# Optimization experiments

Hardware: AMD Instinct MI355X
Metric: run time of the kernel (lower is better)

## Reference

```python
import math
import jax, jax.numpy as jnp
import numpy as np

B, N, ND, CD, H, L, T = 2, 384, 8, 16, 128, 4, 100

def silu(x):
    return x * jax.nn.sigmoid(x)

def mlp2(x, w1, b1, w2, b2):
    return silu(x @ w1 + b1) @ w2 + b2

def setup_inputs() -> dict:
    key = jax.random.key(0)
    ks = iter(jax.random.split(key, 80))
    def nrm(shape, scale=1.0):
        return jax.random.normal(next(ks), shape, jnp.float32) * scale
    def lin(fi, fo):
        s = 1.0 / np.sqrt(fi)
        return nrm((fi, fo), s), nrm((fo,), s)
    def stack_lin(fi, fo):
        ws, bs = zip(*[lin(fi, fo) for _ in range(L)])
        return jnp.stack(ws), jnp.stack(bs)
    inp = {}
    inp['node_features'] = nrm((B, N, ND))
    inp['positions'] = nrm((B, N, 2))
    inp['mask'] = jnp.ones((B, N), jnp.float32)
    inp['condition'] = nrm((B, CD))
    inp['targets'] = nrm((B, 4))
    inp['property_weights'] = jax.random.uniform(next(ks), (4,), jnp.float32)
    inp['feature_noise'] = nrm((B, N, ND))
    inp['position_noise'] = nrm((B, N, 2))
    inp['timesteps'] = jax.random.randint(next(ks), (B,), 0, T)
    inp['time_w1'], inp['time_b1'] = lin(H, H)
    inp['time_w2'], inp['time_b2'] = lin(H, H)
    inp['cond_w1'], inp['cond_b1'] = lin(CD, H)
    inp['cond_w2'], inp['cond_b2'] = lin(H, H)
    inp['nodep_w1'], inp['nodep_b1'] = lin(ND + 2, H)
    inp['nodep_w2'], inp['nodep_b2'] = lin(H, H)
    inp['edge_w1'], inp['edge_b1'] = stack_lin(2 * H + 1, H)
    inp['edge_w2'], inp['edge_b2'] = stack_lin(H, H)
    inp['nodem_w1'], inp['nodem_b1'] = stack_lin(2 * H, H)
    inp['nodem_w2'], inp['nodem_b2'] = stack_lin(H, H)
    inp['feat_w1'], inp['feat_b1'] = lin(H, H)
    inp['feat_w2'], inp['feat_b2'] = lin(H, ND)
    inp['pos_w1'], inp['pos_b1'] = lin(H, H)
    inp['pos_w2'], inp['pos_b2'] = lin(H, 2)
    inp['prop_w1'], inp['prop_b1'] = lin(H, H)
    inp['prop_w2'], inp['prop_b2'] = lin(H, H // 2)
    inp['prop_w3'], inp['prop_b3'] = lin(H // 2, 4)
    return inp

def reference(node_features, positions, mask, condition, targets, property_weights,
              feature_noise, position_noise, timesteps,
              time_w1, time_b1, time_w2, time_b2,
              cond_w1, cond_b1, cond_w2, cond_b2,
              nodep_w1, nodep_b1, nodep_w2, nodep_b2,
              edge_w1, edge_b1, edge_w2, edge_b2,
              nodem_w1, nodem_b1, nodem_w2, nodem_b2,
              feat_w1, feat_b1, feat_w2, feat_b2,
              pos_w1, pos_b1, pos_w2, pos_b2,
              prop_w1, prop_b1, prop_w2, prop_b2, prop_w3, prop_b3):
    # diffusion schedule buffers
    betas = jnp.linspace(1e-4, 0.02, T)
    alpha_bars = jnp.cumprod(1.0 - betas)
    ab = alpha_bars[timesteps][:, None, None]
    nf = jnp.sqrt(ab) * node_features + jnp.sqrt(1.0 - ab) * feature_noise
    npos = jnp.sqrt(ab) * positions + jnp.sqrt(1.0 - ab) * position_noise
    # sinusoidal time embedding
    half = H // 2
    factor = math.log(10000.0) / (half - 1)
    freqs = jnp.exp(jnp.arange(half) * (-factor))
    te = timesteps.astype(jnp.float32)[:, None] * freqs[None, :]
    temb = jnp.concatenate([jnp.sin(te), jnp.cos(te)], -1)
    state = (mlp2(jnp.concatenate([nf, npos], -1), nodep_w1, nodep_b1, nodep_w2, nodep_b2)
             + mlp2(temb, time_w1, time_b1, time_w2, time_b2)[:, None, :]
             + mlp2(condition, cond_w1, cond_b1, cond_w2, cond_b2)[:, None, :])
    # pairwise distances (fixed across layers); eps for grad-safe sqrt at diagonal
    rel = npos[:, :, None, :] - npos[:, None, :, :]
    dist = jnp.sqrt(jnp.sum(rel * rel, -1) + 1e-12)  # [B,N,N]
    emask = mask[:, :, None] * mask[:, None, :]       # [B,N,N]
    denom = jnp.clip(emask.sum(2), 1.0)[..., None]    # [B,N,1]
    mask3 = mask[..., None]

    def layer(s, p):
        ew1, eb1, ew2, eb2, nw1, nb1, nw2, nb2 = p
        # split first edge-linear: cat([node_i, node_j, dist]) @ ew1
        ai = s @ ew1[:H]            # [B,N,H] (i contribution)
        aj = s @ ew1[H:2 * H]       # [B,N,H] (j contribution)
        h = silu(ai[:, :, None, :] + aj[:, None, :, :] + dist[..., None] * ew1[2 * H] + eb1)
        msg = (h @ ew2 + eb2) * emask[..., None]
        agg = msg.sum(2) / denom    # [B,N,H]
        upd = silu(s @ nw1[:H] + agg @ nw1[H:] + nb1) @ nw2 + nb2
        return s + upd * mask3, None

    state, _ = jax.lax.scan(layer, state,
                            (edge_w1, edge_b1, edge_w2, edge_b2,
                             nodem_w1, nodem_b1, nodem_w2, nodem_b2))
    pred_fn = mlp2(state, feat_w1, feat_b1, feat_w2, feat_b2)
    pred_pn = mlp2(state, pos_w1, pos_b1, pos_w2, pos_b2)
    gemb = (state * mask3).sum(1) / jnp.clip(mask.sum(1, keepdims=True), 1.0)
    props = silu(silu(gemb @ prop_w1 + prop_b1) @ prop_w2 + prop_b2) @ prop_w3 + prop_b3
    msum = jnp.clip(mask.sum(), 1.0)
    floss = (((pred_fn - feature_noise) ** 2) * mask3).sum() / msum
    ploss = (((pred_pn - position_noise) ** 2) * mask3).sum() / msum
    noise_loss = floss + ploss
    prop_loss = (((props - targets) ** 2) * property_weights).mean()
    total_loss = noise_loss + prop_loss
    return jnp.stack([noise_loss, prop_loss, total_loss])
```

## Files before the change

kernel.cpp:

```cpp
#include <hip/hip_runtime.h>
#include <math.h>

#define BB 2
#define NN 384
#define ND 8
#define CD 16
#define HH 128
#define LL 4
#define TT 100
#define TOTN (BB * NN)

__device__ __forceinline__ float silu_f(float x) {
    float s = 1.0f / (1.0f + __expf(-x));
    return x * s;
}

__global__ void k_prep(const float* __restrict__ mask, const float* __restrict__ condition,
                       const int* __restrict__ timesteps,
                       const float* __restrict__ time_w1, const float* __restrict__ time_b1,
                       const float* __restrict__ time_w2, const float* __restrict__ time_b2,
                       const float* __restrict__ cond_w1, const float* __restrict__ cond_b1,
                       const float* __restrict__ cond_w2, const float* __restrict__ cond_b2,
                       float* __restrict__ tc, float* __restrict__ scal, float* __restrict__ accums) {
    int b = blockIdx.x;
    int t = threadIdx.x;
    __shared__ float sh[HH];
    __shared__ float sh2[HH];
    __shared__ float shc[CD];
    __shared__ float red[HH];

    if (b == 0 && t < 2) accums[t] = 0.0f;

    int ts = timesteps[b];
    float ab = 1.0f;
    for (int k = 0; k <= ts; ++k) {
        float beta = 1e-4f + (0.02f - 1e-4f) * ((float)k / (float)(TT - 1));
        ab *= (1.0f - beta);
    }
    if (t == 0) {
        scal[b * 4 + 0] = sqrtf(ab);
        scal[b * 4 + 1] = sqrtf(1.0f - ab);
    }
    float m = 0.0f;
    for (int j = t; j < NN; j += HH) m += mask[b * NN + j];
    red[t] = m;
    __syncthreads();
    for (int s = 64; s > 0; s >>= 1) {
        if (t < s) red[t] += red[t + s];
        __syncthreads();
    }
    if (t == 0) scal[b * 4 + 2] = red[0];

    const int half = HH / 2;
    float factor = logf(10000.0f) / (float)(half - 1);
    float tf = (float)ts;
    float temb;
    if (t < half) temb = sinf(tf * __expf(-factor * (float)t));
    else          temb = cosf(tf * __expf(-factor * (float)(t - half)));
    sh[t] = temb;
    if (t < CD) shc[t] = condition[b * CD + t];
    __syncthreads();

    float acc = time_b1[t];
    for (int k = 0; k < HH; ++k) acc += sh[k] * time_w1[k * HH + t];
    sh2[t] = silu_f(acc);
    __syncthreads();
    float acc2 = time_b2[t];
    for (int k = 0; k < HH; ++k) acc2 += sh2[k] * time_w2[k * HH + t];
    float acc3 = cond_b1[t];
    for (int k = 0; k < CD; ++k) acc3 += shc[k] * cond_w1[k * HH + t];
    __syncthreads();
    sh[t] = silu_f(acc3);
    __syncthreads();
    float acc4 = cond_b2[t];
    for (int k = 0; k < HH; ++k) acc4 += sh[k] * cond_w2[k * HH + t];

    tc[b * HH + t] = acc2 + acc4;
}

__global__ __launch_bounds__(256) void k_node_init(
    const float* __restrict__ node_features, const float* __restrict__ positions,
    const float* __restrict__ feature_noise, const float* __restrict__ position_noise,
    const float* __restrict__ nodep_w1, const float* __restrict__ nodep_b1,
    const float* __restrict__ nodep_w2, const float* __restrict__ nodep_b2,
    const float* __restrict__ tc, const float* __restrict__ scal,
    const float* __restrict__ ew1_0, const float* __restrict__ eb1_0,
    float* __restrict__ state, float* __restrict__ npos,
    float* __restrict__ ai0, float* __restrict__ aj0) {
    const int tid = threadIdx.x;
    const int t = tid & 127;
    const int g = tid >> 7;
    const int b0 = blockIdx.x * 4;
    const int b = b0 / NN;

    __shared__ __align__(16) float x[4][12];
    __shared__ __align__(16) float sh1[4][HH];
    __shared__ __align__(16) float sst[4][HH];
    __shared__ float sred[4][2][HH];

    if (tid < 40) {
        int n = tid / 10, c = tid % 10;
        int gn = b0 + n;
        float sab = scal[b * 4 + 0], s1ab = scal[b * 4 + 1];
        float v;
        if (c < ND) {
            v = sab * node_features[gn * ND + c] + s1ab * feature_noise[gn * ND + c];
        } else {
            int d = c - ND;
            v = sab * positions[gn * 2 + d] + s1ab * position_noise[gn * 2 + d];
            npos[gn * 2 + d] = v;
        }
        x[n][c] = v;
    }
    __syncthreads();

    for (int n = 2 * g; n <= 2 * g + 1; ++n) {
        float a = nodep_b1[t];
        #pragma unroll
        for (int k = 0; k < ND + 2; ++k) a += x[n][k] * nodep_w1[k * HH + t];
        sh1[n][t] = silu_f(a);
    }
    __syncthreads();

    {
        float a0 = 0, a1 = 0, a2 = 0, a3 = 0;
        const int k0 = g * 64;
        const float* wr = nodep_w2 + (size_t)k0 * HH + t;
        for (int kk = 0; kk < 64; kk += 4) {
            float w0 = wr[(kk + 0) * HH], w1 = wr[(kk + 1) * HH];
            float w2 = wr[(kk + 2) * HH], w3 = wr[(kk + 3) * HH];
            float4 s;
            s = *(const float4*)&sh1[0][k0 + kk]; a0 += s.x * w0 + s.y * w1 + s.z * w2 + s.w * w3;
            s = *(const float4*)&sh1[1][k0 + kk]; a1 += s.x * w0 + s.y * w1 + s.z * w2 + s.w * w3;
            s = *(const float4*)&sh1[2][k0 + kk]; a2 += s.x * w0 + s.y * w1 + s.z * w2 + s.w * w3;
            s = *(const float4*)&sh1[3][k0 + kk]; a3 += s.x * w0 + s.y * w1 + s.z * w2 + s.w * w3;
        }
        sred[0][g][t] = a0; sred[1][g][t] = a1; sred[2][g][t] = a2; sred[3][g][t] = a3;
    }
    __syncthreads();
    {
        float tcv = nodep_b2[t] + tc[b * HH + t];
        for (int n = 2 * g; n <= 2 * g + 1; ++n) {
            float st = sred[n][0][t] + sred[n][1][t] + tcv;
            state[(size_t)(b0 + n) * HH + t] = st;
            sst[n][t] = st;
        }
    }
    __syncthreads();

    {
        float a0 = 0, a1 = 0, a2 = 0, a3 = 0;
        const int k0 = g * 64;
        const float* wr = ew1_0 + (size_t)k0 * HH + t;
        for (int kk = 0; kk < 64; kk += 4) {
            float w0 = wr[(kk + 0) * HH], w1 = wr[(kk + 1) * HH];
            float w2 = wr[(kk + 2) * HH], w3 = wr[(kk + 3) * HH];
            float4 s;
            s = *(const float4*)&sst[0][k0 + kk]; a0 += s.x * w0 + s.y * w1 + s.z * w2 + s.w * w3;
            s = *(const float4*)&sst[1][k0 + kk]; a1 += s.x * w0 + s.y * w1 + s.z * w2 + s.w * w3;
            s = *(const float4*)&sst[2][k0 + kk]; a2 += s.x * w0 + s.y * w1 + s.z * w2 + s.w * w3;
            s = *(const float4*)&sst[3][k0 + kk]; a3 += s.x * w0 + s.y * w1 + s.z * w2 + s.w * w3;
        }
        sred[0][g][t] = a0; sred[1][g][t] = a1; sred[2][g][t] = a2; sred[3][g][t] = a3;
    }
    __syncthreads();
    for (int n = 2 * g; n <= 2 * g + 1; ++n)
        ai0[(size_t)(b0 + n) * HH + t] = sred[n][0][t] + sred[n][1][t] + eb1_0[t];
    __syncthreads();
    {
        float a0 = 0, a1 = 0, a2 = 0, a3 = 0;
        const int k0 = g * 64;
        const float* wr = ew1_0 + (size_t)(HH + k0) * HH + t;
        for (int kk = 0; kk < 64; kk += 4) {
            float w0 = wr[(kk + 0) * HH], w1 = wr[(kk + 1) * HH];
            float w2 = wr[(kk + 2) * HH], w3 = wr[(kk + 3) * HH];
            float4 s;
            s = *(const float4*)&sst[0][k0 + kk]; a0 += s.x * w0 + s.y * w1 + s.z * w2 + s.w * w3;
            s = *(const float4*)&sst[1][k0 + kk]; a1 += s.x * w0 + s.y * w1 + s.z * w2 + s.w * w3;
            s = *(const float4*)&sst[2][k0 + kk]; a2 += s.x * w0 + s.y * w1 + s.z * w2 + s.w * w3;
            s = *(const float4*)&sst[3][k0 + kk]; a3 += s.x * w0 + s.y * w1 + s.z * w2 + s.w * w3;
        }
        sred[0][g][t] = a0; sred[1][g][t] = a1; sred[2][g][t] = a2; sred[3][g][t] = a3;
    }
    __syncthreads();
    for (int n = 2 * g; n <= 2 * g + 1; ++n)
        aj0[(size_t)(b0 + n) * HH + t] = sred[n][0][t] + sred[n][1][t];
}

__global__ void k_dist(const float* __restrict__ npos, float* __restrict__ dist) {
    int idx = blockIdx.x * blockDim.x + threadIdx.x;
    if (idx >= BB * NN * NN) return;
    int b = idx / (NN * NN);
    int r = idx % (NN * NN);
    int i = r / NN, j = r % NN;
    float dx = npos[(b * NN + i) * 2 + 0] - npos[(b * NN + j) * 2 + 0];
    float dy = npos[(b * NN + i) * 2 + 1] - npos[(b * NN + j) * 2 + 1];
    dist[idx] = sqrtf(dx * dx + dy * dy + 1e-12f);
}

__global__ __launch_bounds__(256) void k_edge(
    const float* __restrict__ ai, const float* __restrict__ aj,
    const float* __restrict__ dist, const float* __restrict__ mask,
    const float* __restrict__ wd, float* __restrict__ Sp) {
    const int tid = threadIdx.x;
    const int t = tid & 127;
    const int g = tid >> 7;
    const int blk = blockIdx.x;
    const int p = blk >> 2, q = blk & 3;
    const int n0 = p * 2, n1 = p * 2 + 1;
    const int b = n0 / NN;
    const int jb = q * 96;

    __shared__ __align__(16) float4 sdm[96];
    __shared__ float sred[2][2][HH];

    for (int i = tid; i < 96; i += 256) {
        int j = jb + i;
        sdm[i] = make_float4(dist[(size_t)n0 * NN + j], dist[(size_t)n1 * NN + j],
                             mask[b * NN + j], 0.0f);
    }
    const float av0 = ai[(size_t)n0 * HH + t];
    const float av1 = ai[(size_t)n1 * HH + t];
    const float wdt = wd[t];
    __syncthreads();

    const float* pa = aj + ((size_t)b * NN + jb) * HH + t;
    float acc0 = 0.0f, acc1 = 0.0f;
    #pragma unroll 4
    for (int i = g; i < 96; i += 2) {
        float4 dm = sdm[i];
        float a = pa[(size_t)i * HH];
        float v0 = av0 + a + dm.x * wdt;
        float v1 = av1 + a + dm.y * wdt;
        acc0 = fmaf(dm.z, silu_f(v0), acc0);
        acc1 = fmaf(dm.z, silu_f(v1), acc1);
    }
    sred[0][g][t] = acc0;
    sred[1][g][t] = acc1;
    __syncthreads();
    if (g == 0) Sp[((size_t)q * TOTN + n0) * HH + t] = sred[0][0][t] + sred[0][1][t];
    else        Sp[((size_t)q * TOTN + n1) * HH + t] = sred[1][0][t] + sred[1][1][t];
}

template<bool LAST>
__global__ __launch_bounds__(256) void k_nodeup(
    const float* __restrict__ Sp, float* __restrict__ state,
    const float* __restrict__ mask, const float* __restrict__ scal,
    const float* __restrict__ ew2, const float* __restrict__ eb2,
    const float* __restrict__ nw1, const float* __restrict__ nb1,
    const float* __restrict__ nw2, const float* __restrict__ nb2,
    const float* __restrict__ ew1n, const float* __restrict__ eb1n,
    float* __restrict__ ai_out, float* __restrict__ aj_out,
    const float* __restrict__ fnoise, const float* __restrict__ pnoise,
    const float* __restrict__ fw1, const float* __restrict__ fb1,
    const float* __restrict__ fw2, const float* __restrict__ fb2,
    const float* __restrict__ pw1, const float* __restrict__ pb1,
    const float* __restrict__ pw2, const float* __restrict__ pb2,
    float* __restrict__ accums, float* __restrict__ gembp) {
    const int tid = threadIdx.x;
    const int t = tid & 127;
    const int g = tid >> 7;
    const int b0 = blockIdx.x * 4;
    const int b = b0 / NN;

    __shared__ __align__(16) float sS[4][HH];
    __shared__ __align__(16) float sst[4][HH];
    __shared__ __align__(16) float sagg[4][HH];
    __shared__ __align__(16) float sh[4][HH];
    __shared__ float sred[4][2][HH];
    __shared__ float lf, lp;

    for (int i = tid; i < 4 * HH; i += 256) {
        int n = i >> 7, tt = i & 127;
        int gn = b0 + n;
        sS[n][tt] = Sp[((size_t)0 * TOTN + gn) * HH + tt] + Sp[((size_t)1 * TOTN + gn) * HH + tt]
                  + Sp[((size_t)2 * TOTN + gn) * HH + tt] + Sp[((size_t)3 * TOTN + gn) * HH + tt];
        sst[n][tt] = state[(size_t)gn * HH + tt];
    }
    if (tid == 0) { lf = 0.0f; lp = 0.0f; }
    __syncthreads();

    {
        float a0 = 0, a1 = 0, a2 = 0, a3 = 0;
        const int k0 = g * 64;
        const float* wr = ew2 + (size_t)k0 * HH + t;
        for (int kk = 0; kk < 64; kk += 4) {
            float w0 = wr[(kk + 0) * HH], w1 = wr[(kk + 1) * HH];
            float w2 = wr[(kk + 2) * HH], w3 = wr[(kk + 3) * HH];
            float4 s;
            s = *(const float4*)&sS[0][k0 + kk]; a0 += s.x * w0 + s.y * w1 + s.z * w2 + s.w * w3;
            s = *(const float4*)&sS[1][k0 + kk]; a1 += s.x * w0 + s.y * w1 + s.z * w2 + s.w * w3;
            s = *(const float4*)&sS[2][k0 + kk]; a2 += s.x * w0 + s.y * w1 + s.z * w2 + s.w * w3;
            s = *(const float4*)&sS[3][k0 + kk]; a3 += s.x * w0 + s.y * w1 + s.z * w2 + s.w * w3;
        }
        sred[0][g][t] = a0; sred[1][g][t] = a1; sred[2][g][t] = a2; sred[3][g][t] = a3;
    }
    __syncthreads();
    {
        const float msum = scal[b * 4 + 2];
        for (int n = 2 * g; n <= 2 * g + 1; ++n) {
            float mi = mask[b0 + n];
            float denom = fmaxf(mi * msum, 1.0f);
            float a = sred[n][0][t] + sred[n][1][t] + msum * eb2[t];
            sagg[n][t] = mi * a / denom;
        }
    }
    __syncthreads();

    {
        float a0 = 0, a1 = 0, a2 = 0, a3 = 0;
        const float* wr = nw1 + (size_t)(g * HH) * HH + t;
        const float (*inp)[HH] = g ? (const float (*)[HH])sagg : (const float (*)[HH])sst;
        for (int kk = 0; kk < HH; kk += 4) {
            float w0 = wr[(kk + 0) * HH], w1 = wr[(kk + 1) * HH];
            float w2 = wr[(kk + 2) * HH], w3 = wr[(kk + 3) * HH];
            float4 s;
            s = *(const float4*)&inp[0][kk]; a0 += s.x * w0 + s.y * w1 + s.z * w2 + s.w * w3;
            s = *(const float4*)&inp[1][kk]; a1 += s.x * w0 + s.y * w1 + s.z * w2 + s.w * w3;
            s = *(const float4*)&inp[2][kk]; a2 += s.x * w0 + s.y * w1 + s.z * w2 + s.w * w3;
            s = *(const float4*)&inp[3][kk]; a3 += s.x * w0 + s.y * w1 + s.z * w2 + s.w * w3;
        }
        sred[0][g][t] = a0; sred[1][g][t] = a1; sred[2][g][t] = a2; sred[3][g][t] = a3;
    }
    __syncthreads();
    for (int n = 2 * g; n <= 2 * g + 1; ++n)
        sh[n][t] = silu_f(sred[n][0][t] + sred[n][1][t] + nb1[t]);
    __syncthreads();

    {
        float a0 = 0, a1 = 0, a2 = 0, a3 = 0;
        const int k0 = g * 64;
        const float* wr = nw2 + (size_t)k0 * HH + t;
        for (int kk = 0; kk < 64; kk += 4) {
            float w0 = wr[(kk + 0) * HH], w1 = wr[(kk + 1) * HH];
            float w2 = wr[(kk + 2) * HH], w3 = wr[(kk + 3) * HH];
            float4 s;
            s = *(const float4*)&sh[0][k0 + kk]; a0 += s.x * w0 + s.y * w1 + s.z * w2 + s.w * w3;
            s = *(const float4*)&sh[1][k0 + kk]; a1 += s.x * w0 + s.y * w1 + s.z * w2 + s.w * w3;
            s = *(const float4*)&sh[2][k0 + kk]; a2 += s.x * w0 + s.y * w1 + s.z * w2 + s.w * w3;
            s = *(const float4*)&sh[3][k0 + kk]; a3 += s.x * w0 + s.y * w1 + s.z * w2 + s.w * w3;
        }
        sred[0][g][t] = a0; sred[1][g][t] = a1; sred[2][g][t] = a2; sred[3][g][t] = a3;
    }
    __syncthreads();
    for (int n = 2 * g; n <= 2 * g + 1; ++n) {
        int gn = b0 + n;
        float mi = mask[gn];
        float ns = sst[n][t] + (sred[n][0][t] + sred[n][1][t] + nb2[t]) * mi;
        state[(size_t)gn * HH + t] = ns;
        sst[n][t] = ns;
    }
    __syncthreads();

    if (!LAST) {
        {
            float a0 = 0, a1 = 0, a2 = 0, a3 = 0;
            const int k0 = g * 64;
            const float* wr = ew1n + (size_t)k0 * HH + t;
            for (int kk = 0; kk < 64; kk += 4) {
                float w0 = wr[(kk + 0) * HH], w1 = wr[(kk + 1) * HH];
                float w2 = wr[(kk + 2) * HH], w3 = wr[(kk + 3) * HH];
                float4 s;
                s = *(const float4*)&sst[0][k0 + kk]; a0 += s.x * w0 + s.y * w1 + s.z * w2 + s.w * w3;
                s = *(const float4*)&sst[1][k0 + kk]; a1 += s.x * w0 + s.y * w1 + s.z * w2 + s.w * w3;
                s = *(const float4*)&sst[2][k0 + kk]; a2 += s.x * w0 + s.y * w1 + s.z * w2 + s.w * w3;
                s = *(const float4*)&sst[3][k0 + kk]; a3 += s.x * w0 + s.y * w1 + s.z * w2 + s.w * w3;
            }
            sred[0][g][t] = a0; sred[1][g][t] = a1; sred[2][g][t] = a2; sred[3][g][t] = a3;
        }
        __syncthreads();
        for (int n = 2 * g; n <= 2 * g + 1; ++n)
            ai_out[(size_t)(b0 + n) * HH + t] = sred[n][0][t] + sred[n][1][t] + eb1n[t];
        __syncthreads();
        {
            float a0 = 0, a1 = 0, a2 = 0, a3 = 0;
            const int k0 = g * 64;
            const float* wr = ew1n + (size_t)(HH + k0) * HH + t;
            for (int kk = 0; kk < 64; kk += 4) {
                float w0 = wr[(kk + 0) * HH], w1 = wr[(kk + 1) * HH];
                float w2 = wr[(kk + 2) * HH], w3 = wr[(kk + 3) * HH];
                float4 s;
                s = *(const float4*)&sst[0][k0 + kk]; a0 += s.x * w0 + s.y * w1 + s.z * w2 + s.w * w3;
                s = *(const float4*)&sst[1][k0 + kk]; a1 += s.x * w0 + s.y * w1 + s.z * w2 + s.w * w3;
                s = *(const float4*)&sst[2][k0 + kk]; a2 += s.x * w0 + s.y * w1 + s.z * w2 + s.w * w3;
                s = *(const float4*)&sst[3][k0 + kk]; a3 += s.x * w0 + s.y * w1 + s.z * w2 + s.w * w3;
            }
            sred[0][g][t] = a0; sred[1][g][t] = a1; sred[2][g][t] = a2; sred[3][g][t] = a3;
        }
        __syncthreads();
        for (int n = 2 * g; n <= 2 * g + 1; ++n)
            aj_out[(size_t)(b0 + n) * HH + t] = sred[n][0][t] + sred[n][1][t];
    } else {
        {
            float a0 = 0, a1 = 0, a2 = 0, a3 = 0;
            const int k0 = g * 64;
            const float* wr = fw1 + (size_t)k0 * HH + t;
            for (int kk = 0; kk < 64; kk += 4) {
                float w0 = wr[(kk + 0) * HH], w1 = wr[(kk + 1) * HH];
                float w2 = wr[(kk + 2) * HH], w3 = wr[(kk + 3) * HH];
                float4 s;
                s = *(const float4*)&sst[0][k0 + kk]; a0 += s.x * w0 + s.y * w1 + s.z * w2 + s.w * w3;
                s = *(const float4*)&sst[1][k0 + kk]; a1 += s.x * w0 + s.y * w1 + s.z * w2 + s.w * w3;
                s = *(const float4*)&sst[2][k0 + kk]; a2 += s.x * w0 + s.y * w1 + s.z * w2 + s.w * w3;
                s = *(const float4*)&sst[3][k0 + kk]; a3 += s.x * w0 + s.y * w1 + s.z * w2 + s.w * w3;
            }
            sred[0][g][t] = a0; sred[1][g][t] = a1; sred[2][g][t] = a2; sred[3][g][t] = a3;
        }
        __syncthreads();
        for (int n = 2 * g; n <= 2 * g + 1; ++n)
            sS[n][t] = silu_f(sred[n][0][t] + sred[n][1][t] + fb1[t]);
        __syncthreads();
        {
            float a0 = 0, a1 = 0, a2 = 0, a3 = 0;
            const int k0 = g * 64;
            const float* wr = pw1 + (size_t)k0 * HH + t;
            for (int kk = 0; kk < 64; kk += 4) {
                float w0 = wr[(kk + 0) * HH], w1 = wr[(kk + 1) * HH];
                float w2 = wr[(kk + 2) * HH], w3 = wr[(kk + 3) * HH];
                float4 s;
                s = *(const float4*)&sst[0][k0 + kk]; a0 += s.x * w0 + s.y * w1 + s.z * w2 + s.w * w3;
                s = *(const float4*)&sst[1][k0 + kk]; a1 += s.x * w0 + s.y * w1 + s.z * w2 + s.w * w3;
                s = *(const float4*)&sst[2][k0 + kk]; a2 += s.x * w0 + s.y * w1 + s.z * w2 + s.w * w3;
                s = *(const float4*)&sst[3][k0 + kk]; a3 += s.x * w0 + s.y * w1 + s.z * w2 + s.w * w3;
            }
            sred[0][g][t] = a0; sred[1][g][t] = a1; sred[2][g][t] = a2; sred[3][g][t] = a3;
        }
        __syncthreads();
        for (int n = 2 * g; n <= 2 * g + 1; ++n)
            sagg[n][t] = silu_f(sred[n][0][t] + sred[n][1][t] + pb1[t]);
        __syncthreads();

        {
            int n = tid >> 6, lane = tid & 63;
            int gn = b0 + n;
            float mi = mask[gn];
            if (lane < ND) {
                float o = fb2[lane];
                for (int k = 0; k < HH; ++k) o += sS[n][k] * fw2[k * ND + lane];
                float d = o - fnoise[(size_t)gn * ND + lane];
                atomicAdd(&lf, mi * d * d);
            } else if (lane < ND + 2) {
                int c = lane - ND;
                float o = pb2[c];
                for (int k = 0; k < HH; ++k) o += sagg[n][k] * pw2[k * 2 + c];
                float d = o - pnoise[(size_t)gn * 2 + c];
                atomicAdd(&lp, mi * d * d);
            }
        }
        {
            float v = sst[2 * g][t] * mask[b0 + 2 * g] + sst[2 * g + 1][t] * mask[b0 + 2 * g + 1];
            sred[0][g][t] = v;
        }
        __syncthreads();
        if (g == 0) gembp[(size_t)blockIdx.x * HH + t] = sred[0][0][t] + sred[0][1][t];
        if (tid == 0) {
            atomicAdd(&accums[0], lf);
            atomicAdd(&accums[1], lp);
        }
    }
}

__global__ void k_final(const float* __restrict__ gembp, const float* __restrict__ targets,
                        const float* __restrict__ pweights,
                        const float* __restrict__ w1, const float* __restrict__ b1,
                        const float* __restrict__ w2, const float* __restrict__ b2,
                        const float* __restrict__ w3, const float* __restrict__ b3,
                        const float* __restrict__ accums, const float* __restrict__ scal,
                        float* __restrict__ out) {
    int t = threadIdx.x;
    __shared__ float g[HH], h1[HH], h2[64];
    __shared__ float ploss_acc;
    if (t == 0) ploss_acc = 0.0f;
    for (int b = 0; b < BB; ++b) {
        __syncthreads();
        float acc = 0.0f;
        const float* gp = gembp + (size_t)b * 96 * HH + t;
        #pragma unroll 8
        for (int r = 0; r < 96; ++r) acc += gp[(size_t)r * HH];
        g[t] = acc / fmaxf(scal[b * 4 + 2], 1.0f);
        __syncthreads();
        float a = b1[t];
        for (int k = 0; k < HH; ++k) a += g[k] * w1[k * HH + t];
        h1[t] = silu_f(a);
        __syncthreads();
        if (t < 64) {
            float a2 = b2[t];
            for (int k = 0; k < HH; ++k) a2 += h1[k] * w2[k * 64 + t];
            h2[t] = silu_f(a2);
        }
        __syncthreads();
        if (t < 4) {
            float o = b3[t];
            for (int k = 0; k < 64; ++k) o += h2[k] * w3[k * 4 + t];
            float d = o - targets[b * 4 + t];
            atomicAdd(&ploss_acc, d * d * pweights[t]);
        }
    }
    __syncthreads();
    if (t == 0) {
        float msumt = fmaxf(scal[0 * 4 + 2] + scal[1 * 4 + 2], 1.0f);
        float noise = (accums[0] + accums[1]) / msumt;
        float prop = ploss_acc / (float)(BB * 4);
        out[0] = noise;
        out[1] = prop;
        out[2] = noise + prop;
    }
}

extern "C" void kernel_launch(void* const* d_in, const int* in_sizes, int n_in,
                              void* d_out, int out_size, void* d_ws, size_t ws_size,
                              hipStream_t stream) {
    const float* node_features  = (const float*)d_in[0];
    const float* positions      = (const float*)d_in[1];
    const float* mask           = (const float*)d_in[2];
    const float* condition     = (const float*)d_in[3];
    const float* targets        = (const float*)d_in[4];
    const float* pweights       = (const float*)d_in[5];
    const float* feature_noise  = (const float*)d_in[6];
    const float* position_noise = (const float*)d_in[7];
    const int*   timesteps      = (const int*)d_in[8];
    const float* time_w1 = (const float*)d_in[9];
    const float* time_b1 = (const float*)d_in[10];
    const float* time_w2 = (const float*)d_in[11];
    const float* time_b2 = (const float*)d_in[12];
    const float* cond_w1 = (const float*)d_in[13];
    const float* cond_b1 = (const float*)d_in[14];
    const float* cond_w2 = (const float*)d_in[15];
    const float* cond_b2 = (const float*)d_in[16];
    const float* nodep_w1 = (const float*)d_in[17];
    const float* nodep_b1 = (const float*)d_in[18];
    const float* nodep_w2 = (const float*)d_in[19];
    const float* nodep_b2 = (const float*)d_in[20];
    const float* edge_w1 = (const float*)d_in[21];
    const float* edge_b1 = (const float*)d_in[22];
    const float* edge_w2 = (const float*)d_in[23];
    const float* edge_b2 = (const float*)d_in[24];
    const float* nodem_w1 = (const float*)d_in[25];
    const float* nodem_b1 = (const float*)d_in[26];
    const float* nodem_w2 = (const float*)d_in[27];
    const float* nodem_b2 = (const float*)d_in[28];
    const float* feat_w1 = (const float*)d_in[29];
    const float* feat_b1 = (const float*)d_in[30];
    const float* feat_w2 = (const float*)d_in[31];
    const float* feat_b2 = (const float*)d_in[32];
    const float* pos_w1 = (const float*)d_in[33];
    const float* pos_b1 = (const float*)d_in[34];
    const float* pos_w2 = (const float*)d_in[35];
    const float* pos_b2 = (const float*)d_in[36];
    const float* prop_w1 = (const float*)d_in[37];
    const float* prop_b1 = (const float*)d_in[38];
    const float* prop_w2 = (const float*)d_in[39];
    const float* prop_b2 = (const float*)d_in[40];
    const float* prop_w3 = (const float*)d_in[41];
    const float* prop_b3 = (const float*)d_in[42];

    float* ws = (float*)d_ws;
    float* npos   = ws;
    float* state  = npos + BB * NN * 2;
    float* dist   = state + TOTN * HH;
    float* aiA    = dist + (size_t)TOTN * NN;
    float* ajA    = aiA + TOTN * HH;
    float* aiB    = ajA + TOTN * HH;
    float* ajB    = aiB + TOTN * HH;
    float* Sp     = ajB + TOTN * HH;
    float* tc     = Sp + 4 * TOTN * HH;
    float* scal   = tc + BB * HH;
    float* accums = scal + BB * 4;
    float* gembp  = accums + 2;

    float* outp = (float*)d_out;

    k_prep<<<BB, HH, 0, stream>>>(mask, condition, timesteps,
                                  time_w1, time_b1, time_w2, time_b2,
                                  cond_w1, cond_b1, cond_w2, cond_b2,
                                  tc, scal, accums);
    k_node_init<<<TOTN / 4, 256, 0, stream>>>(node_features, positions, feature_noise, position_noise,
                                              nodep_w1, nodep_b1, nodep_w2, nodep_b2,
                                              tc, scal, edge_w1, edge_b1, state, npos, aiA, ajA);
    k_dist<<<(BB * NN * NN + 255) / 256, 256, 0, stream>>>(npos, dist);

    for (int l = 0; l < LL; ++l) {
        const float* ew1l = edge_w1 + (size_t)l * (2 * HH + 1) * HH;
        const float* wd   = ew1l + (size_t)(2 * HH) * HH;
        const float* ew2  = edge_w2 + (size_t)l * HH * HH;
        const float* eb2  = edge_b2 + (size_t)l * HH;
        const float* nw1  = nodem_w1 + (size_t)l * 2 * HH * HH;
        const float* nb1  = nodem_b1 + (size_t)l * HH;
        const float* nw2  = nodem_w2 + (size_t)l * HH * HH;
        const float* nb2  = nodem_b2 + (size_t)l * HH;
        const float* ew1n = edge_w1 + (size_t)(l + 1) * (2 * HH + 1) * HH;
        const float* eb1n = edge_b1 + (size_t)(l + 1) * HH;

        const float* ai_in = (l & 1) ? aiB : aiA;
        const float* aj_in = (l & 1) ? ajB : ajA;
        float* ai_out = (l & 1) ? aiA : aiB;
        float* aj_out = (l & 1) ? ajA : ajB;

        k_edge<<<TOTN / 2 * 4, 256, 0, stream>>>(ai_in, aj_in, dist, mask, wd, Sp);

        if (l < LL - 1) {
            k_nodeup<false><<<TOTN / 4, 256, 0, stream>>>(
                Sp, state, mask, scal, ew2, eb2, nw1, nb1, nw2, nb2, ew1n, eb1n,
                ai_out, aj_out,
                feature_noise, position_noise, feat_w1, feat_b1, feat_w2, feat_b2,
                pos_w1, pos_b1, pos_w2, pos_b2, accums, gembp);
        } else {
            k_nodeup<true><<<TOTN / 4, 256, 0, stream>>>(
                Sp, state, mask, scal, ew2, eb2, nw1, nb1, nw2, nb2, ew1n, eb1n,
                ai_out, aj_out,
                feature_noise, position_noise, feat_w1, feat_b1, feat_w2, feat_b2,
                pos_w1, pos_b1, pos_w2, pos_b2, accums, gembp);
        }
    }

    k_final<<<1, HH, 0, stream>>>(gembp, targets, pweights,
                                  prop_w1, prop_b1, prop_w2, prop_b2, prop_w3, prop_b3,
                                  accums, scal, outp);
}
```

Measured before the change: 334.4 us.

## Split node-update work across more blocks and threads; parallelize final head over batch

k_nodeup now handles 2 nodes per block with 512 threads, where it used to handle 4 nodes with 256. Each GEMV's K dimension is split four ways and reduced through shared memory, which doubles the grid and shortens each thread's serial loop. k_final now processes both batch elements at once with 256 threads instead of looping over them. The cost is that weight matrices are re-read by twice as many blocks, and the extra reduction adds shared-memory traffic.

After: 320.1 us. -4.3%, faster.

```diff
diff --git a/kernel.cpp b/kernel.cpp
--- a/kernel.cpp
+++ b/kernel.cpp
@@ -243,7 +243,7 @@
 }
 
 template<bool LAST>
-__global__ __launch_bounds__(256) void k_nodeup(
+__global__ __launch_bounds__(512) void k_nodeup(
     const float* __restrict__ Sp, float* __restrict__ state,
     const float* __restrict__ mask, const float* __restrict__ scal,
     const float* __restrict__ ew2, const float* __restrict__ eb2,
@@ -260,18 +260,18 @@
     const int tid = threadIdx.x;
     const int t = tid & 127;
     const int g = tid >> 7;
-    const int b0 = blockIdx.x * 4;
+    const int b0 = blockIdx.x * 2;
     const int b = b0 / NN;
 
-    __shared__ __align__(16) float sS[4][HH];
-    __shared__ __align__(16) float sst[4][HH];
-    __shared__ __align__(16) float sagg[4][HH];
-    __shared__ __align__(16) float sh[4][HH];
-    __shared__ float sred[4][2][HH];
+    __shared__ __align__(16) float sS[2][HH];
+    __shared__ __align__(16) float sst[2][HH];
+    __shared__ __align__(16) float sagg[2][HH];
+    __shared__ __align__(16) float sh[2][HH];
+    __shared__ float sred[2][4][HH];
     __shared__ float lf, lp;
 
-    for (int i = tid; i < 4 * HH; i += 256) {
-        int n = i >> 7, tt = i & 127;
+    if (tid < 2 * HH) {
+        int n = tid >> 7, tt = tid & 127;
         int gn = b0 + n;
         sS[n][tt] = Sp[((size_t)0 * TOTN + gn) * HH + tt] + Sp[((size_t)1 * TOTN + gn) * HH + tt]
                   + Sp[((size_t)2 * TOTN + gn) * HH + tt] + Sp[((size_t)3 * TOTN + gn) * HH + tt];
@@ -281,156 +281,139 @@
     __syncthreads();
 
     {
-        float a0 = 0, a1 = 0, a2 = 0, a3 = 0;
-        const int k0 = g * 64;
+        float a0 = 0, a1 = 0;
+        const int k0 = g * 32;
         const float* wr = ew2 + (size_t)k0 * HH + t;
-        for (int kk = 0; kk < 64; kk += 4) {
+        for (int kk = 0; kk < 32; kk += 4) {
             float w0 = wr[(kk + 0) * HH], w1 = wr[(kk + 1) * HH];
             float w2 = wr[(kk + 2) * HH], w3 = wr[(kk + 3) * HH];
             float4 s;
             s = *(const float4*)&sS[0][k0 + kk]; a0 += s.x * w0 + s.y * w1 + s.z * w2 + s.w * w3;
             s = *(const float4*)&sS[1][k0 + kk]; a1 += s.x * w0 + s.y * w1 + s.z * w2 + s.w * w3;
-            s = *(const float4*)&sS[2][k0 + kk]; a2 += s.x * w0 + s.y * w1 + s.z * w2 + s.w * w3;
-            s = *(const float4*)&sS[3][k0 + kk]; a3 += s.x * w0 + s.y * w1 + s.z * w2 + s.w * w3;
-        }
-        sred[0][g][t] = a0; sred[1][g][t] = a1; sred[2][g][t] = a2; sred[3][g][t] = a3;
-    }
-    __syncthreads();
+        }
+        sred[0][g][t] = a0; sred[1][g][t] = a1;
+    }
+    __syncthreads();
+    if (g < 2) {
+        const float msum = scal[b * 4 + 2];
+        float mi = mask[b0 + g];
+        float denom = fmaxf(mi * msum, 1.0f);
+        float a = sred[g][0][t] + sred[g][1][t] + sred[g][2][t] + sred[g][3][t] + msum * eb2[t];
+        sagg[g][t] = mi * a / denom;
+    }
+    __syncthreads();
+
     {
-        const float msum = scal[b * 4 + 2];
-        for (int n = 2 * g; n <= 2 * g + 1; ++n) {
-            float mi = mask[b0 + n];
-            float denom = fmaxf(mi * msum, 1.0f);
-            float a = sred[n][0][t] + sred[n][1][t] + msum * eb2[t];
-            sagg[n][t] = mi * a / denom;
-        }
-    }
-    __syncthreads();
-
-    {
-        float a0 = 0, a1 = 0, a2 = 0, a3 = 0;
-        const float* wr = nw1 + (size_t)(g * HH) * HH + t;
-        const float (*inp)[HH] = g ? (const float (*)[HH])sagg : (const float (*)[HH])sst;
-        for (int kk = 0; kk < HH; kk += 4) {
+        float a0 = 0, a1 = 0;
+        const int r0 = g * 64;
+        const float* wr = nw1 + (size_t)r0 * HH + t;
+        const float (*inp)[HH] = (g < 2) ? (const float (*)[HH])sst : (const float (*)[HH])sagg;
+        const int rb = (g & 1) * 64;
+        for (int kk = 0; kk < 64; kk += 4) {
             float w0 = wr[(kk + 0) * HH], w1 = wr[(kk + 1) * HH];
             float w2 = wr[(kk + 2) * HH], w3 = wr[(kk + 3) * HH];
             float4 s;
-            s = *(const float4*)&inp[0][kk]; a0 += s.x * w0 + s.y * w1 + s.z * w2 + s.w * w3;
-            s = *(const float4*)&inp[1][kk]; a1 += s.x * w0 + s.y * w1 + s.z * w2 + s.w * w3;
-            s = *(const float4*)&inp[2][kk]; a2 += s.x * w0 + s.y * w1 + s.z * w2 + s.w * w3;
-            s = *(const float4*)&inp[3][kk]; a3 += s.x * w0 + s.y * w1 + s.z * w2 + s.w * w3;
-        }
-        sred[0][g][t] = a0; sred[1][g][t] = a1; sred[2][g][t] = a2; sred[3][g][t] = a3;
-    }
-    __syncthreads();
-    for (int n = 2 * g; n <= 2 * g + 1; ++n)
-        sh[n][t] = silu_f(sred[n][0][t] + sred[n][1][t] + nb1[t]);
+            s = *(const float4*)&inp[0][rb + kk]; a0 += s.x * w0 + s.y * w1 + s.z * w2 + s.w * w3;
+            s = *(const float4*)&inp[1][rb + kk]; a1 += s.x * w0 + s.y * w1 + s.z * w2 + s.w * w3;
+        }
+        sred[0][g][t] = a0; sred[1][g][t] = a1;
+    }
+    __syncthreads();
+    if (g < 2) sh[g][t] = silu_f(sred[g][0][t] + sred[g][1][t] + sred[g][2][t] + sred[g][3][t] + nb1[t]);
     __syncthreads();
 
     {
-        float a0 = 0, a1 = 0, a2 = 0, a3 = 0;
-        const int k0 = g * 64;
+        float a0 = 0, a1 = 0;
+        const int k0 = g * 32;
         const float* wr = nw2 + (size_t)k0 * HH + t;
-        for (int kk = 0; kk < 64; kk += 4) {
+        for (int kk = 0; kk < 32; kk += 4) {
             float w0 = wr[(kk + 0) * HH], w1 = wr[(kk + 1) * HH];
             float w2 = wr[(kk + 2) * HH], w3 = wr[(kk + 3) * HH];
             float4 s;
             s = *(const float4*)&sh[0][k0 + kk]; a0 += s.x * w0 + s.y * w1 + s.z * w2 + s.w * w3;
             s = *(const float4*)&sh[1][k0 + kk]; a1 += s.x * w0 + s.y * w1 + s.z * w2 + s.w * w3;
-            s = *(const float4*)&sh[2][k0 + kk]; a2 += s.x * w0 + s.y * w1 + s.z * w2 + s.w * w3;
-            s = *(const float4*)&sh[3][k0 + kk]; a3 += s.x * w0 + s.y * w1 + s.z * w2 + s.w * w3;
-        }
-        sred[0][g][t] = a0; sred[1][g][t] = a1; sred[2][g][t] = a2; sred[3][g][t] = a3;
-    }
-    __syncthreads();
-    for (int n = 2 * g; n <= 2 * g + 1; ++n) {
-        int gn = b0 + n;
+        }
+        sred[0][g][t] = a0; sred[1][g][t] = a1;
+    }
+    __syncthreads();
+    if (g < 2) {
+        int gn = b0 + g;
         float mi = mask[gn];
-        float ns = sst[n][t] + (sred[n][0][t] + sred[n][1][t] + nb2[t]) * mi;
+        float ns = sst[g][t] + (sred[g][0][t] + sred[g][1][t] + sred[g][2][t] + sred[g][3][t] + nb2[t]) * mi;
         state[(size_t)gn * HH + t] = ns;
-        sst[n][t] = ns;
+        sst[g][t] = ns;
     }
     __syncthreads();
 
     if (!LAST) {
         {
-            float a0 = 0, a1 = 0, a2 = 0, a3 = 0;
-            const int k0 = g * 64;
+            float a0 = 0, a1 = 0;
+            const int k0 = g * 32;
             const float* wr = ew1n + (size_t)k0 * HH + t;
-            for (int kk = 0; kk < 64; kk += 4) {
+            for (int kk = 0; kk < 32; kk += 4) {
                 float w0 = wr[(kk + 0) * HH], w1 = wr[(kk + 1) * HH];
                 float w2 = wr[(kk + 2) * HH], w3 = wr[(kk + 3) * HH];
                 float4 s;
                 s = *(const float4*)&sst[0][k0 + kk]; a0 += s.x * w0 + s.y * w1 + s.z * w2 + s.w * w3;
                 s = *(const float4*)&sst[1][k0 + kk]; a1 += s.x * w0 + s.y * w1 + s.z * w2 + s.w * w3;
-                s = *(const float4*)&sst[2][k0 + kk]; a2 += s.x * w0 + s.y * w1 + s.z * w2 + s.w * w3;
-                s = *(const float4*)&sst[3][k0 + kk]; a3 += s.x * w0 + s.y * w1 + s.z * w2 + s.w * w3;
             }
-            sred[0][g][t] = a0; sred[1][g][t] = a1; sred[2][g][t] = a2; sred[3][g][t] = a3;
-        }
-        __syncthreads();
-        for (int n = 2 * g; n <= 2 * g + 1; ++n)
-            ai_out[(size_t)(b0 + n) * HH + t] = sred[n][0][t] + sred[n][1][t] + eb1n[t];
+            sred[0][g][t] = a0; sred[1][g][t] = a1;
+        }
+        __syncthreads();
+        if (g < 2) ai_out[(size_t)(b0 + g) * HH + t] =
+            sred[g][0][t] + sred[g][1][t] + sred[g][2][t] + sred[g][3][t] + eb1n[t];
         __syncthreads();
         {
-            float a0 = 0, a1 = 0, a2 = 0, a3 = 0;
-            const int k0 = g * 64;
+            float a0 = 0, a1 = 0;
+            const int k0 = g * 32;
             const float* wr = ew1n + (size_t)(HH + k0) * HH + t;
-            for (int kk = 0; kk < 64; kk += 4) {
+            for (int kk = 0; kk < 32; kk += 4) {
                 float w0 = wr[(kk + 0) * HH], w1 = wr[(kk + 1) * HH];
                 float w2 = wr[(kk + 2) * HH], w3 = wr[(kk + 3) * HH];
                 float4 s;
                 s = *(const float4*)&sst[0][k0 + kk]; a0 += s.x * w0 + s.y * w1 + s.z * w2 + s.w * w3;
                 s = *(const float4*)&sst[1][k0 + kk]; a1 += s.x * w0 + s.y * w1 + s.z * w2 + s.w * w3;
-                s = *(const float4*)&sst[2][k0 + kk]; a2 += s.x * w0 + s.y * w1 + s.z * w2 + s.w * w3;
-                s = *(const float4*)&sst[3][k0 + kk]; a3 += s.x * w0 + s.y * w1 + s.z * w2 + s.w * w3;
             }
-            sred[0][g][t] = a0; sred[1][g][t] = a1; sred[2][g][t] = a2; sred[3][g][t] = a3;
-        }
-        __syncthreads();
-        for (int n = 2 * g; n <= 2 * g + 1; ++n)
-            aj_out[(size_t)(b0 + n) * HH + t] = sred[n][0][t] + sred[n][1][t];
+            sred[0][g][t] = a0; sred[1][g][t] = a1;
+        }
+        __syncthreads();
+        if (g < 2) aj_out[(size_t)(b0 + g) * HH + t] =
+            sred[g][0][t] + sred[g][1][t] + sred[g][2][t] + sred[g][3][t];
     } else {
         {
-            float a0 = 0, a1 = 0, a2 = 0, a3 = 0;
-            const int k0 = g * 64;
+            float a0 = 0, a1 = 0;
+            const int k0 = g * 32;
             const float* wr = fw1 + (size_t)k0 * HH + t;
-            for (int kk = 0; kk < 64; kk += 4) {
+            for (int kk = 0; kk < 32; kk += 4) {
                 float w0 = wr[(kk + 0) * HH], w1 = wr[(kk + 1) * HH];
                 float w2 = wr[(kk + 2) * HH], w3 = wr[(kk + 3) * HH];
                 float4 s;
                 s = *(const float4*)&sst[0][k0 + kk]; a0 += s.x * w0 + s.y * w1 + s.z * w2 + s.w * w3;
                 s = *(const float4*)&sst[1][k0 + kk]; a1 += s.x * w0 + s.y * w1 + s.z * w2 + s.w * w3;
-                s = *(const float4*)&sst[2][k0 + kk]; a2 += s.x * w0 + s.y * w1 + s.z * w2 + s.w * w3;
-                s = *(const float4*)&sst[3][k0 + kk]; a3 += s.x * w0 + s.y * w1 + s.z * w2 + s.w * w3;
             }
-            sred[0][g][t] = a0; sred[1][g][t] = a1; sred[2][g][t] = a2; sred[3][g][t] = a3;
-        }
-        __syncthreads();
-        for (int n = 2 * g; n <= 2 * g + 1; ++n)
-            sS[n][t] = silu_f(sred[n][0][t] + sred[n][1][t] + fb1[t]);
+            sred[0][g][t] = a0; sred[1][g][t] = a1;
+        }
+        __syncthreads();
+        if (g < 2) sS[g][t] = silu_f(sred[g][0][t] + sred[g][1][t] + sred[g][2][t] + sred[g][3][t] + fb1[t]);
         __syncthreads();
         {
-            float a0 = 0, a1 = 0, a2 = 0, a3 = 0;
-            const int k0 = g * 64;
+            float a0 = 0, a1 = 0;
+            const int k0 = g * 32;
             const float* wr = pw1 + (size_t)k0 * HH + t;
-            for (int kk = 0; kk < 64; kk += 4) {
+            for (int kk = 0; kk < 32; kk += 4) {
                 float w0 = wr[(kk + 0) * HH], w1 = wr[(kk + 1) * HH];
                 float w2 = wr[(kk + 2) * HH], w3 = wr[(kk + 3) * HH];
                 float4 s;
                 s = *(const float4*)&sst[0][k0 + kk]; a0 += s.x * w0 + s.y * w1 + s.z * w2 + s.w * w3;
                 s = *(const float4*)&sst[1][k0 + kk]; a1 += s.x * w0 + s.y * w1 + s.z * w2 + s.w * w3;
-                s = *(const float4*)&sst[2][k0 + kk]; a2 += s.x * w0 + s.y * w1 + s.z * w2 + s.w * w3;
-                s = *(const float4*)&sst[3][k0 + kk]; a3 += s.x * w0 + s.y * w1 + s.z * w2 + s.w * w3;
             }
-            sred[0][g][t] = a0; sred[1][g][t] = a1; sred[2][g][t] = a2; sred[3][g][t] = a3;
-        }
-        __syncthreads();
-        for (int n = 2 * g; n <= 2 * g + 1; ++n)
-            sagg[n][t] = silu_f(sred[n][0][t] + sred[n][1][t] + pb1[t]);
-        __syncthreads();
-
-        {
+            sred[0][g][t] = a0; sred[1][g][t] = a1;
+        }
+        __syncthreads();
+        if (g < 2) sagg[g][t] = silu_f(sred[g][0][t] + sred[g][1][t] + sred[g][2][t] + sred[g][3][t] + pb1[t]);
+        __syncthreads();
+
+        if (tid < 128) {
             int n = tid >> 6, lane = tid & 63;
             int gn = b0 + n;
             float mi = mask[gn];
@@ -447,12 +430,11 @@
                 atomicAdd(&lp, mi * d * d);
             }
         }
-        {
-            float v = sst[2 * g][t] * mask[b0 + 2 * g] + sst[2 * g + 1][t] * mask[b0 + 2 * g + 1];
-            sred[0][g][t] = v;
-        }
-        __syncthreads();
-        if (g == 0) gembp[(size_t)blockIdx.x * HH + t] = sred[0][0][t] + sred[0][1][t];
+        if (g == 0) {
+            float v = sst[0][t] * mask[b0] + sst[1][t] * mask[b0 + 1];
+            gembp[(size_t)blockIdx.x * HH + t] = v;
+        }
+        __syncthreads();
         if (tid == 0) {
             atomicAdd(&accums[0], lf);
             atomicAdd(&accums[1], lp);
@@ -460,47 +442,49 @@
     }
 }
 
-__global__ void k_final(const float* __restrict__ gembp, const float* __restrict__ targets,
-                        const float* __restrict__ pweights,
-                        const float* __restrict__ w1, const float* __restrict__ b1,
-                        const float* __restrict__ w2, const float* __restrict__ b2,
-                        const float* __restrict__ w3, const float* __restrict__ b3,
-                        const float* __restrict__ accums, const float* __restrict__ scal,
-                        float* __restrict__ out) {
-    int t = threadIdx.x;
-    __shared__ float g[HH], h1[HH], h2[64];
-    __shared__ float ploss_acc;
-    if (t == 0) ploss_acc = 0.0f;
-    for (int b = 0; b < BB; ++b) {
-        __syncthreads();
-        float acc = 0.0f;
-        const float* gp = gembp + (size_t)b * 96 * HH + t;
-        #pragma unroll 8
-        for (int r = 0; r < 96; ++r) acc += gp[(size_t)r * HH];
-        g[t] = acc / fmaxf(scal[b * 4 + 2], 1.0f);
-        __syncthreads();
-        float a = b1[t];
-        for (int k = 0; k < HH; ++k) a += g[k] * w1[k * HH + t];
-        h1[t] = silu_f(a);
-        __syncthreads();
-        if (t < 64) {
-            float a2 = b2[t];
-            for (int k = 0; k < HH; ++k) a2 += h1[k] * w2[k * 64 + t];
-            h2[t] = silu_f(a2);
-        }
-        __syncthreads();
-        if (t < 4) {
-            float o = b3[t];
-            for (int k = 0; k < 64; ++k) o += h2[k] * w3[k * 4 + t];
-            float d = o - targets[b * 4 + t];
-            atomicAdd(&ploss_acc, d * d * pweights[t]);
-        }
-    }
-    __syncthreads();
-    if (t == 0) {
+__global__ __launch_bounds__(256) void k_final(
+    const float* __restrict__ gembp, const float* __restrict__ targets,
+    const float* __restrict__ pweights,
+    const float* __restrict__ w1, const float* __restrict__ b1,
+    const float* __restrict__ w2, const float* __restrict__ b2,
+    const float* __restrict__ w3, const float* __restrict__ b3,
+    const float* __restrict__ accums, const float* __restrict__ scal,
+    float* __restrict__ out) {
+    const int tid = threadIdx.x;
+    const int t = tid & 127;
+    const int b = tid >> 7;
+    __shared__ float g2[BB][HH], h1[BB][HH], h2[BB][64];
+    __shared__ float pl;
+    if (tid == 0) pl = 0.0f;
+
+    float acc = 0.0f;
+    const float* gp = gembp + (size_t)b * 192 * HH + t;
+    #pragma unroll 8
+    for (int r = 0; r < 192; ++r) acc += gp[(size_t)r * HH];
+    g2[b][t] = acc / fmaxf(scal[b * 4 + 2], 1.0f);
+    __syncthreads();
+
+    float a = b1[t];
+    for (int k = 0; k < HH; ++k) a += g2[b][k] * w1[k * HH + t];
+    h1[b][t] = silu_f(a);
+    __syncthreads();
+    if (t < 64) {
+        float a2 = b2[t];
+        for (int k = 0; k < HH; ++k) a2 += h1[b][k] * w2[k * 64 + t];
+        h2[b][t] = silu_f(a2);
+    }
+    __syncthreads();
+    if (t < 4) {
+        float o = b3[t];
+        for (int k = 0; k < 64; ++k) o += h2[b][k] * w3[k * 4 + t];
+        float d = o - targets[b * 4 + t];
+        atomicAdd(&pl, d * d * pweights[t]);
+    }
+    __syncthreads();
+    if (tid == 0) {
         float msumt = fmaxf(scal[0 * 4 + 2] + scal[1 * 4 + 2], 1.0f);
         float noise = (accums[0] + accums[1]) / msumt;
-        float prop = ploss_acc / (float)(BB * 4);
+        float prop = pl / (float)(BB * 4);
         out[0] = noise;
         out[1] = prop;
         out[2] = noise + prop;
@@ -599,13 +583,13 @@
         k_edge<<<TOTN / 2 * 4, 256, 0, stream>>>(ai_in, aj_in, dist, mask, wd, Sp);
 
         if (l < LL - 1) {
-            k_nodeup<false><<<TOTN / 4, 256, 0, stream>>>(
+            k_nodeup<false><<<TOTN / 2, 512, 0, stream>>>(
                 Sp, state, mask, scal, ew2, eb2, nw1, nb1, nw2, nb2, ew1n, eb1n,
                 ai_out, aj_out,
                 feature_noise, position_noise, feat_w1, feat_b1, feat_w2, feat_b2,
                 pos_w1, pos_b1, pos_w2, pos_b2, accums, gembp);
         } else {
-            k_nodeup<true><<<TOTN / 4, 256, 0, stream>>>(
+            k_nodeup<true><<<TOTN / 2, 512, 0, stream>>>(
                 Sp, state, mask, scal, ew2, eb2, nw1, nb1, nw2, nb2, ew1n, eb1n,
                 ai_out, aj_out,
                 feature_noise, position_noise, feat_w1, feat_b1, feat_w2, feat_b2,
@@ -613,7 +597,7 @@
         }
     }
 
-    k_final<<<1, HH, 0, stream>>>(gembp, targets, pweights,
-                                  prop_w1, prop_b1, prop_w2, prop_b2, prop_w3, prop_b3,
-                                  accums, scal, outp);
-}
+    k_final<<<1, 256, 0, stream>>>(gembp, targets, pweights,
+                                   prop_w1, prop_b1, prop_w2, prop_b2, prop_w3, prop_b3,
+                                   accums, scal, outp);
+}
```
